# Kernel tuning notes

Measured on AMD Instinct MI355X. Metric: run time of the kernel, lower is better.

Reference implementation:

```python
import jax, jax.numpy as jnp
import numpy as np

N = 100000
E = 1600000
IN_C, HID_C, OUT_C = 128, 128, 64
EPS = 1e-5


def setup_inputs() -> dict:
    key = jax.random.key(0)
    ks = jax.random.split(key, 12)
    x = jax.random.normal(ks[0], (N, IN_C), dtype=jnp.float32)
    edge_index = jax.random.randint(ks[1], (2, E), 0, N, dtype=jnp.int64)
    def lin(k, fan_in, fan_out):
        s = 1.0 / np.sqrt(fan_in)
        return jax.random.uniform(k, (fan_in, fan_out), jnp.float32, -s, s)
    return {
        "x": x,
        "W1": lin(ks[2], IN_C, HID_C), "b1": jnp.zeros((HID_C,), jnp.float32),
        "g1": jnp.ones((HID_C,), jnp.float32), "be1": jnp.zeros((HID_C,), jnp.float32),
        "W2": lin(ks[3], HID_C, HID_C), "b2": jnp.zeros((HID_C,), jnp.float32),
        "g2": jnp.ones((HID_C,), jnp.float32), "be2": jnp.zeros((HID_C,), jnp.float32),
        "W3": lin(ks[4], HID_C, OUT_C), "b3": jnp.zeros((OUT_C,), jnp.float32),
        "edge_index": edge_index,
    }


def gcn_conv(x, W, b, src, dst, dinv):
    # x' = D^{-1/2}(A+I)D^{-1/2} (x W) + b ; src/dst already include self loops
    h = x @ W                                    # [N, C_out]
    norm = dinv[src] * dinv[dst]                 # [E+N]
    msg = h[src] * norm[:, None]                 # [E+N, C_out] (memory-bound gather)
    out = jax.ops.segment_sum(msg, dst, num_segments=N)
    return out + b


def batchnorm_relu(h, gamma, beta):
    # training-mode BatchNorm1d: batch stats over nodes, biased variance
    mean = jnp.mean(h, axis=0)
    var = jnp.mean((h - mean) ** 2, axis=0)
    y = gamma * (h - mean) * jax.lax.rsqrt(var + EPS) + beta
    return jax.nn.relu(y)


def reference(x, W1, b1, g1, be1, W2, b2, g2, be2, W3, b3, edge_index):
    loop = jnp.arange(N, dtype=edge_index.dtype)
    src = jnp.concatenate([edge_index[0], loop])
    dst = jnp.concatenate([edge_index[1], loop])
    deg = jax.ops.segment_sum(jnp.ones_like(dst, dtype=jnp.float32), dst, num_segments=N)
    dinv = jax.lax.rsqrt(jnp.maximum(deg, 1.0))

    h = gcn_conv(x, W1, b1, src, dst, dinv)
    h = batchnorm_relu(h, g1, be1)
    h = gcn_conv(h, W2, b2, src, dst, dinv)
    h = batchnorm_relu(h, g2, be2)
    out = gcn_conv(h, W3, b3, src, dst, dinv)
    return (h, out)
```

## Files before the change

### kernel.cpp

```cpp
#include <hip/hip_runtime.h>
#include <hip/hip_bf16.h>

#define NNODES 100000
#define NEDGES 1600000
#define EPSBN 1e-5f

#define BKT_SHIFT 9
#define NODES_PER_BKT 512
#define NBKT 196
#define NCHUNK 256
#define CHUNK 6250
#define SRC_MASK 0x1FFFF
#define NSLOT 64

typedef unsigned short u16;
typedef unsigned int u32;
typedef __bf16 bf16x8 __attribute__((ext_vector_type(8)));
typedef float floatx4 __attribute__((ext_vector_type(4)));
typedef unsigned int uint4v __attribute__((ext_vector_type(4)));
typedef float float4v __attribute__((ext_vector_type(4)));

__device__ __forceinline__ u16 f2bf(float f) {
    unsigned int u = __float_as_uint(f);
    unsigned int r = (u + 0x7fffu + ((u >> 16) & 1u)) >> 16;
    return (u16)r;
}
__device__ __forceinline__ float bflo(unsigned int u) { return __uint_as_float(u << 16); }
__device__ __forceinline__ float bfhi(unsigned int u) { return __uint_as_float(u & 0xffff0000u); }

__device__ __forceinline__ void nt_store_u4(void* p, uint4 v) {
    uint4v t; t.x = v.x; t.y = v.y; t.z = v.z; t.w = v.w;
    __builtin_nontemporal_store(t, (uint4v*)p);
}
__device__ __forceinline__ void nt_store_f4(float* p, float4 v) {
    float4v t; t.x = v.x; t.y = v.y; t.z = v.z; t.w = v.w;
    __builtin_nontemporal_store(t, (float4v*)p);
}


__global__ __launch_bounds__(256) void k_hist(const int* __restrict__ ei, int* __restrict__ histT) {
    __shared__ int h[NBKT];
    int tid = threadIdx.x;
    if (tid < NBKT) h[tid] = 0;
    __syncthreads();
    int base = blockIdx.x * CHUNK;
    for (int e = base + tid; e < base + CHUNK; e += 256) {
        int d = ei[NEDGES + e];
        atomicAdd(&h[d >> BKT_SHIFT], 1);
    }
    __syncthreads();
    if (tid < NBKT) histT[tid * NCHUNK + blockIdx.x] = h[tid];
}

__global__ __launch_bounds__(256) void k_bbase(const int* __restrict__ histT, int* __restrict__ bbase,
                                               int* __restrict__ rowptr) {
    __shared__ int sdata[256];
    int tid = threadIdx.x;
    int s = 0;
    if (tid < NBKT) {
        for (int g = 0; g < NCHUNK; ++g) s += histT[tid * NCHUNK + g];
    }
    int val = s;
    sdata[tid] = val;
    __syncthreads();
    for (int off = 1; off < 256; off <<= 1) {
        int add = (tid >= off) ? sdata[tid - off] : 0;
        __syncthreads();
        val += add;
        sdata[tid] = val;
        __syncthreads();
    }
    if (tid < NBKT) bbase[tid] = val - s;
    if (tid == 0) { bbase[NBKT] = NEDGES; rowptr[NNODES] = NEDGES; }
}

__global__ __launch_bounds__(256) void k_bscan(const int* __restrict__ histT, const int* __restrict__ bbase,
                                               int* __restrict__ offT) {
    __shared__ int sdata[256];
    int b = blockIdx.x;
    int g = threadIdx.x;
    int v = histT[b * NCHUNK + g];
    int val = v;
    sdata[g] = val;
    __syncthreads();
    for (int off = 1; off < 256; off <<= 1) {
        int add = (g >= off) ? sdata[g - off] : 0;
        __syncthreads();
        val += add;
        sdata[g] = val;
        __syncthreads();
    }
    offT[b * NCHUNK + g] = bbase[b] + (val - v);
}

__global__ __launch_bounds__(256) void k_scatter(const int* __restrict__ ei, const int* __restrict__ offT,
                                                 u32* __restrict__ rec) {
    __shared__ int cur[NBKT];
    int tid = threadIdx.x;
    if (tid < NBKT) cur[tid] = offT[tid * NCHUNK + blockIdx.x];
    __syncthreads();
    int base = blockIdx.x * CHUNK;
    for (int e = base + tid; e < base + CHUNK; e += 256) {
        int s = ei[e];
        int d = ei[NEDGES + e];
        int b = d >> BKT_SHIFT;
        int p = atomicAdd(&cur[b], 1);
        rec[p] = ((u32)(d & (NODES_PER_BKT - 1)) << 17) | (u32)s;
    }
}

__global__ __launch_bounds__(256) void k_bfill(const u32* __restrict__ rec, const int* __restrict__ bbase,
                                               int* __restrict__ rowptr, float* __restrict__ dinv,
                                               int* __restrict__ colsrc) {
    __shared__ int cnt[NODES_PER_BKT];
    __shared__ int sdata[256];
    int tid = threadIdx.x;
    int b = blockIdx.x;
    int n0 = b * NODES_PER_BKT;
    int r0 = bbase[b], r1 = bbase[b + 1];
    cnt[2 * tid] = 0;
    cnt[2 * tid + 1] = 0;
    __syncthreads();
    for (int r = r0 + tid; r < r1; r += 256) {
        atomicAdd(&cnt[rec[r] >> 17], 1);
    }
    __syncthreads();
    int c0 = cnt[2 * tid], c1 = cnt[2 * tid + 1];
    int ps = c0 + c1;
    int val = ps;
    sdata[tid] = val;
    __syncthreads();
    for (int off = 1; off < 256; off <<= 1) {
        int add = (tid >= off) ? sdata[tid - off] : 0;
        __syncthreads();
        val += add;
        sdata[tid] = val;
        __syncthreads();
    }
    int e0 = val - ps;
    int e1 = e0 + c0;
    int na = n0 + 2 * tid, nb2 = n0 + 2 * tid + 1;
    if (na < NNODES) {
        rowptr[na] = r0 + e0;
        dinv[na] = rsqrtf((float)(c0 + 1));
    }
    if (nb2 < NNODES) {
        rowptr[nb2] = r0 + e1;
        dinv[nb2] = rsqrtf((float)(c1 + 1));
    }
    cnt[2 * tid] = r0 + e0;
    cnt[2 * tid + 1] = r0 + e1;
    __syncthreads();
    for (int r = r0 + tid; r < r1; r += 256) {
        u32 u = rec[r];
        int p = atomicAdd(&cnt[u >> 17], 1);
        colsrc[p] = (int)(u & SRC_MASK);
    }
}


template <int COUT>
__device__ __forceinline__ void packone(const float* __restrict__ W, u16* __restrict__ Wp, int f) {
    constexpr int CT = COUT / 16;
    if (f >= 4 * CT * 64) return;
    int ks = f / (CT * 64);
    int ct = (f / 64) % CT;
    int lane = f % 64;
    int quad = lane >> 4, mm = lane & 15;
#pragma unroll
    for (int j = 0; j < 8; ++j) {
        float v = W[(size_t)(ks * 32 + quad * 8 + j) * COUT + ct * 16 + mm];
        Wp[(size_t)f * 8 + j] = f2bf(v);
    }
}

__global__ __launch_bounds__(256) void k_packW_all(const float* __restrict__ W1, const float* __restrict__ W2,
                                                   const float* __restrict__ W3, u16* __restrict__ Wp1,
                                                   u16* __restrict__ Wp2, u16* __restrict__ Wp3) {
    int b = blockIdx.x;
    if (b < 8) packone<128>(W1, Wp1, b * 256 + threadIdx.x);
    else if (b < 16) packone<128>(W2, Wp2, (b - 8) * 256 + threadIdx.x);
    else packone<64>(W3, Wp3, (b - 16) * 256 + threadIdx.x);
}


template <int COUT, bool AFFINE, bool WRITEH, bool BF16IN>
__global__ __launch_bounds__(256) void k_mfma_gemm(const void* __restrict__ Xv, const u16* __restrict__ Wp,
                                                   const float* __restrict__ dinv,
                                                   const float* __restrict__ scale, const float* __restrict__ shift,
                                                   u16* __restrict__ Bout, float* __restrict__ Hout) {
    constexpr int CT = COUT / 16;
    const int wave = threadIdx.x >> 6;
    const int lane = threadIdx.x & 63;
    const int quad = lane >> 4;
    const int m = lane & 15;
    const int rowbase = blockIdx.x * 64 + wave * 16;
    const int arow = rowbase + m;
    const bool rv = arow < NNODES;
    floatx4 acc[CT];
#pragma unroll
    for (int ct = 0; ct < CT; ++ct) acc[ct] = floatx4{0.f, 0.f, 0.f, 0.f};
#pragma unroll
    for (int ks = 0; ks < 4; ++ks) {
        const int k0 = ks * 32 + quad * 8;
        float4 xa = make_float4(0.f, 0.f, 0.f, 0.f), xb = xa;
        if (rv) {
            if (BF16IN) {
                uint4 q = *(const uint4*)((const u16*)Xv + (size_t)arow * 128 + k0);
                xa.x = bflo(q.x); xa.y = bfhi(q.x); xa.z = bflo(q.y); xa.w = bfhi(q.y);
                xb.x = bflo(q.z); xb.y = bfhi(q.z); xb.z = bflo(q.w); xb.w = bfhi(q.w);
            } else {
                xa = *(const float4*)((const float*)Xv + (size_t)arow * 128 + k0);
                xb = *(const float4*)((const float*)Xv + (size_t)arow * 128 + k0 + 4);
            }
        }
        if (AFFINE) {
            float4 sa = *(const float4*)(scale + k0), sb = *(const float4*)(scale + k0 + 4);
            float4 ha = *(const float4*)(shift + k0), hb = *(const float4*)(shift + k0 + 4);
            xa.x = fmaxf(fmaf(xa.x, sa.x, ha.x), 0.f);
            xa.y = fmaxf(fmaf(xa.y, sa.y, ha.y), 0.f);
            xa.z = fmaxf(fmaf(xa.z, sa.z, ha.z), 0.f);
            xa.w = fmaxf(fmaf(xa.w, sa.w, ha.w), 0.f);
            xb.x = fmaxf(fmaf(xb.x, sb.x, hb.x), 0.f);
            xb.y = fmaxf(fmaf(xb.y, sb.y, hb.y), 0.f);
            xb.z = fmaxf(fmaf(xb.z, sb.z, hb.z), 0.f);
            xb.w = fmaxf(fmaf(xb.w, sb.w, hb.w), 0.f);
        }
        if (WRITEH && rv) {
            nt_store_f4(Hout + (size_t)arow * 128 + k0, xa);
            nt_store_f4(Hout + (size_t)arow * 128 + k0 + 4, xb);
        }
        union { u16 h[8]; bf16x8 v; } ua;
        ua.h[0] = f2bf(xa.x); ua.h[1] = f2bf(xa.y); ua.h[2] = f2bf(xa.z); ua.h[3] = f2bf(xa.w);
        ua.h[4] = f2bf(xb.x); ua.h[5] = f2bf(xb.y); ua.h[6] = f2bf(xb.z); ua.h[7] = f2bf(xb.w);
#pragma unroll
        for (int ct = 0; ct < CT; ++ct) {
            uint4 bv = *(const uint4*)(Wp + ((size_t)(ks * CT + ct) * 64 + lane) * 8);
            bf16x8 b = *(const bf16x8*)&bv;
            acc[ct] = __builtin_amdgcn_mfma_f32_16x16x32_bf16(ua.v, b, acc[ct], 0, 0, 0);
        }
    }
    float dv[4];
#pragma unroll
    for (int reg = 0; reg < 4; ++reg) {
        int r = rowbase + quad * 4 + reg;
        dv[reg] = (r < NNODES) ? dinv[r] : 0.f;
    }
#pragma unroll
    for (int ct = 0; ct < CT; ++ct) {
#pragma unroll
        for (int reg = 0; reg < 4; ++reg) {
            int r = rowbase + quad * 4 + reg;
            if (r < NNODES) Bout[(size_t)r * COUT + ct * 16 + m] = f2bf(dv[reg] * acc[ct][reg]);
        }
    }
}


template <bool STATS, bool OUTB>
__global__ __launch_bounds__(256) void k_agg128v(const u16* __restrict__ Bm, const float* __restrict__ dinv,
                                                 const int* __restrict__ rowptr, const int* __restrict__ colsrc,
                                                 const float* __restrict__ bias, void* __restrict__ Outv,
                                                 float* __restrict__ slots) {
    __shared__ float sO[4][128];
    const int wave = threadIdx.x >> 6;
    const int node = blockIdx.x * 4 + wave;
    const int lane = threadIdx.x & 63;
    const int g = lane >> 4;
    const int c16 = lane & 15;
    const uint4* Bq = (const uint4*)Bm;
    float a0[8], a1[8];
#pragma unroll
    for (int j = 0; j < 8; ++j) { a0[j] = 0.f; a1[j] = 0.f; }
    const int beg = rowptr[node];
    const int L = rowptr[node + 1] - beg + 1;
    for (int it = 0; it < L; it += 8) {
        int i0 = it + g, i1 = it + 4 + g;
        float w0 = (i0 < L) ? 1.f : 0.f;
        float w1 = (i1 < L) ? 1.f : 0.f;
        i0 = min(i0, L - 1);
        i1 = min(i1, L - 1);
        int s0 = colsrc[beg + max(i0, 1) - 1];
        int s1 = colsrc[beg + max(i1, 1) - 1];
        if (i0 == 0) s0 = node;
        uint4 q0 = Bq[(size_t)s0 * 16 + c16];
        uint4 q1 = Bq[(size_t)s1 * 16 + c16];
        a0[0] += w0 * bflo(q0.x); a0[1] += w0 * bfhi(q0.x);
        a0[2] += w0 * bflo(q0.y); a0[3] += w0 * bfhi(q0.y);
        a0[4] += w0 * bflo(q0.z); a0[5] += w0 * bfhi(q0.z);
        a0[6] += w0 * bflo(q0.w); a0[7] += w0 * bfhi(q0.w);
        a1[0] += w1 * bflo(q1.x); a1[1] += w1 * bfhi(q1.x);
        a1[2] += w1 * bflo(q1.y); a1[3] += w1 * bfhi(q1.y);
        a1[4] += w1 * bflo(q1.z); a1[5] += w1 * bfhi(q1.z);
        a1[6] += w1 * bflo(q1.w); a1[7] += w1 * bfhi(q1.w);
    }
    const float dv = dinv[node];
    float o[8];
#pragma unroll
    for (int j = 0; j < 8; ++j) {
        float s = a0[j] + a1[j];
        s += __shfl_xor(s, 16);
        s += __shfl_xor(s, 32);
        o[j] = dv * s + bias[c16 * 8 + j];
    }
    if (g == 0) {
        if (OUTB) {
            u16* OutB = (u16*)Outv;
            union { u32 w[4]; uint4 q; } p;
            p.w[0] = (u32)f2bf(o[0]) | ((u32)f2bf(o[1]) << 16);
            p.w[1] = (u32)f2bf(o[2]) | ((u32)f2bf(o[3]) << 16);
            p.w[2] = (u32)f2bf(o[4]) | ((u32)f2bf(o[5]) << 16);
            p.w[3] = (u32)f2bf(o[6]) | ((u32)f2bf(o[7]) << 16);
            nt_store_u4(OutB + (size_t)node * 128 + c16 * 8, p.q);
        } else {
            float* Out = (float*)Outv;
            nt_store_f4(Out + (size_t)node * 128 + c16 * 8, make_float4(o[0], o[1], o[2], o[3]));
            nt_store_f4(Out + (size_t)node * 128 + c16 * 8 + 4, make_float4(o[4], o[5], o[6], o[7]));
        }
        if (STATS) {
#pragma unroll
            for (int j = 0; j < 8; ++j) sO[wave][c16 * 8 + j] = o[j];
        }
    }
    if (STATS) {
        __syncthreads();
        if (threadIdx.x < 128) {
            float s = 0.f, q = 0.f;
#pragma unroll
            for (int wv = 0; wv < 4; ++wv) {
                float v = sO[wv][threadIdx.x];
                s += v;
                q += v * v;
            }
            float* slot = slots + (size_t)(blockIdx.x & (NSLOT - 1)) * 256;
            atomicAdd(&slot[threadIdx.x], s);
            atomicAdd(&slot[128 + threadIdx.x], q);
        }
    }
}

__global__ __launch_bounds__(256) void k_agg64v(const u16* __restrict__ Bm, const float* __restrict__ dinv,
                                                const int* __restrict__ rowptr, const int* __restrict__ colsrc,
                                                const float* __restrict__ bias, float* __restrict__ Out) {
    const int node = blockIdx.x * 4 + (threadIdx.x >> 6);
    const int lane = threadIdx.x & 63;
    const int g = lane >> 3;
    const int c8 = lane & 7;
    const uint4* Bq = (const uint4*)Bm;
    float a0[8], a1[8];
#pragma unroll
    for (int j = 0; j < 8; ++j) { a0[j] = 0.f; a1[j] = 0.f; }
    const int beg = rowptr[node];
    const int L = rowptr[node + 1] - beg + 1;
    for (int it = 0; it < L; it += 16) {
        int i0 = it + g, i1 = it + 8 + g;
        float w0 = (i0 < L) ? 1.f : 0.f;
        float w1 = (i1 < L) ? 1.f : 0.f;
        i0 = min(i0, L - 1);
        i1 = min(i1, L - 1);
        int s0 = colsrc[beg + max(i0, 1) - 1];
        int s1 = colsrc[beg + max(i1, 1) - 1];
        if (i0 == 0) s0 = node;
        uint4 q0 = Bq[(size_t)s0 * 8 + c8];
        uint4 q1 = Bq[(size_t)s1 * 8 + c8];
        a0[0] += w0 * bflo(q0.x); a0[1] += w0 * bfhi(q0.x);
        a0[2] += w0 * bflo(q0.y); a0[3] += w0 * bfhi(q0.y);
        a0[4] += w0 * bflo(q0.z); a0[5] += w0 * bfhi(q0.z);
        a0[6] += w0 * bflo(q0.w); a0[7] += w0 * bfhi(q0.w);
        a1[0] += w1 * bflo(q1.x); a1[1] += w1 * bfhi(q1.x);
        a1[2] += w1 * bflo(q1.y); a1[3] += w1 * bfhi(q1.y);
        a1[4] += w1 * bflo(q1.z); a1[5] += w1 * bfhi(q1.z);
        a1[6] += w1 * bflo(q1.w); a1[7] += w1 * bfhi(q1.w);
    }
    const float dv = dinv[node];
    float o[8];
#pragma unroll
    for (int j = 0; j < 8; ++j) {
        float s = a0[j] + a1[j];
        s += __shfl_xor(s, 8);
        s += __shfl_xor(s, 16);
        s += __shfl_xor(s, 32);
        o[j] = dv * s + bias[c8 * 8 + j];
    }
    if (g == 0) {
        nt_store_f4(Out + (size_t)node * 64 + c8 * 8, make_float4(o[0], o[1], o[2], o[3]));
        nt_store_f4(Out + (size_t)node * 64 + c8 * 8 + 4, make_float4(o[4], o[5], o[6], o[7]));
    }
}


__global__ void k_bn_final(const float* __restrict__ slots, const float* __restrict__ g,
                           const float* __restrict__ be, float* __restrict__ scale, float* __restrict__ shift) {
    int c = threadIdx.x;
    float s = 0.f, q = 0.f;
    for (int k = 0; k < NSLOT; ++k) {
        s += slots[(size_t)k * 256 + c];
        q += slots[(size_t)k * 256 + 128 + c];
    }
    float mean = s * (1.0f / NNODES);
    float var = q * (1.0f / NNODES) - mean * mean;
    float istd = rsqrtf(var + EPSBN);
    float sc = g[c] * istd;
    scale[c] = sc;
    shift[c] = be[c] - sc * mean;
}


extern "C" void kernel_launch(void* const* d_in, const int* in_sizes, int n_in,
                              void* d_out, int out_size, void* d_ws, size_t ws_size,
                              hipStream_t stream) {
    const float* x   = (const float*)d_in[0];
    const float* W1  = (const float*)d_in[1];
    const float* b1  = (const float*)d_in[2];
    const float* g1  = (const float*)d_in[3];
    const float* be1 = (const float*)d_in[4];
    const float* W2  = (const float*)d_in[5];
    const float* b2  = (const float*)d_in[6];
    const float* g2  = (const float*)d_in[7];
    const float* be2 = (const float*)d_in[8];
    const float* W3  = (const float*)d_in[9];
    const float* b3  = (const float*)d_in[10];
    const int* ei    = (const int*)d_in[11];

    float* out_h = (float*)d_out;
    float* out_o = (float*)d_out + (size_t)NNODES * 128;

    char* w = (char*)d_ws;
    u16* A16 = (u16*)w;        w += (size_t)NNODES * 128 * 2;
    u16* Bm = (u16*)w;         w += (size_t)NNODES * 128 * 2;
    float* dinv = (float*)w;   w += (size_t)NNODES * 4;
    int* rowptr = (int*)w;     w += (size_t)(NNODES + 32) * 4;
    int* colsrc = (int*)w;     w += (size_t)(NEDGES + 8) * 4;
    int* bbase = (int*)w;      w += (NBKT + 4) * 4;
    float* slots1 = (float*)w; w += (size_t)NSLOT * 256 * 4;
    float* slots2 = (float*)w; w += (size_t)NSLOT * 256 * 4;
    float* scale = (float*)w;  w += 128 * 4;
    float* shift = (float*)w;  w += 128 * 4;
    u16* Wp1 = (u16*)w;        w += 128 * 128 * 2;
    u16* Wp2 = (u16*)w;        w += 128 * 128 * 2;
    u16* Wp3 = (u16*)w;        w += 128 * 64 * 2;

    u32* rec  = (u32*)A16;
    int* histT = (int*)Bm;
    int* offT  = (int*)Bm + NBKT * NCHUNK;

    hipMemsetAsync(slots1, 0, (size_t)2 * NSLOT * 256 * 4, stream);

    k_packW_all<<<20, 256, 0, stream>>>(W1, W2, W3, Wp1, Wp2, Wp3);

    k_hist<<<NCHUNK, 256, 0, stream>>>(ei, histT);
    k_bbase<<<1, 256, 0, stream>>>(histT, bbase, rowptr);
    k_bscan<<<NBKT, 256, 0, stream>>>(histT, bbase, offT);
    k_scatter<<<NCHUNK, 256, 0, stream>>>(ei, offT, rec);
    k_bfill<<<NBKT, 256, 0, stream>>>(rec, bbase, rowptr, dinv, colsrc);

    const int GB = (NNODES + 63) / 64;
    const int AB = NNODES / 4;

    k_mfma_gemm<128, false, false, false><<<GB, 256, 0, stream>>>(x, Wp1, dinv, nullptr, nullptr, Bm, nullptr);
    k_agg128v<true, true><<<AB, 256, 0, stream>>>(Bm, dinv, rowptr, colsrc, b1, A16, slots1);
    k_bn_final<<<1, 128, 0, stream>>>(slots1, g1, be1, scale, shift);

    k_mfma_gemm<128, true, false, true><<<GB, 256, 0, stream>>>(A16, Wp2, dinv, scale, shift, Bm, nullptr);
    k_agg128v<true, true><<<AB, 256, 0, stream>>>(Bm, dinv, rowptr, colsrc, b2, A16, slots2);
    k_bn_final<<<1, 128, 0, stream>>>(slots2, g2, be2, scale, shift);

    k_mfma_gemm<64, true, true, true><<<GB, 256, 0, stream>>>(A16, Wp3, dinv, scale, shift, Bm, out_h);
    k_agg64v<<<AB, 256, 0, stream>>>(Bm, dinv, rowptr, colsrc, b3, out_o);
}
```

Baseline: 463.5 us.

## Split 128-wide aggregation into two 64-column halves per block

The 128-channel aggregation kernel now launches twice as many blocks. Each block handles one 64-column half for four nodes, and the two halves of a node group sit in adjacent block IDs so they can share cache for the gathered rows. Each wave now processes 16 edges per iteration instead of 8, which is meant to raise memory-level parallelism on the gather. Index loads from colsrc are made nontemporal. In exchange, colsrc and rowptr are read twice and there are more BN-stat atomics per node.

```diff
diff --git a/kernel.cpp b/kernel.cpp
--- a/kernel.cpp
+++ b/kernel.cpp
@@ -258,33 +258,37 @@
 
 
 template <bool STATS, bool OUTB>
-__global__ __launch_bounds__(256) void k_agg128v(const u16* __restrict__ Bm, const float* __restrict__ dinv,
+__global__ __launch_bounds__(256) void k_agg128h(const u16* __restrict__ Bm, const float* __restrict__ dinv,
                                                  const int* __restrict__ rowptr, const int* __restrict__ colsrc,
                                                  const float* __restrict__ bias, void* __restrict__ Outv,
                                                  float* __restrict__ slots) {
-    __shared__ float sO[4][128];
+    __shared__ float sO[4][64];
+    const int bid = blockIdx.x;
+    const int half = (bid & 7) >> 2;
+    const int nodeblk = (bid >> 3) * 4 + (bid & 3);
     const int wave = threadIdx.x >> 6;
-    const int node = blockIdx.x * 4 + wave;
+    const int node = nodeblk * 4 + wave;
     const int lane = threadIdx.x & 63;
-    const int g = lane >> 4;
-    const int c16 = lane & 15;
+    const int g = lane >> 3;
+    const int c8 = lane & 7;
     const uint4* Bq = (const uint4*)Bm;
+    const int hoff = half * 8 + c8;
     float a0[8], a1[8];
 #pragma unroll
     for (int j = 0; j < 8; ++j) { a0[j] = 0.f; a1[j] = 0.f; }
     const int beg = rowptr[node];
     const int L = rowptr[node + 1] - beg + 1;
-    for (int it = 0; it < L; it += 8) {
-        int i0 = it + g, i1 = it + 4 + g;
+    for (int it = 0; it < L; it += 16) {
+        int i0 = it + g, i1 = it + 8 + g;
         float w0 = (i0 < L) ? 1.f : 0.f;
         float w1 = (i1 < L) ? 1.f : 0.f;
         i0 = min(i0, L - 1);
         i1 = min(i1, L - 1);
-        int s0 = colsrc[beg + max(i0, 1) - 1];
-        int s1 = colsrc[beg + max(i1, 1) - 1];
+        int s0 = __builtin_nontemporal_load(&colsrc[beg + max(i0, 1) - 1]);
+        int s1 = __builtin_nontemporal_load(&colsrc[beg + max(i1, 1) - 1]);
         if (i0 == 0) s0 = node;
-        uint4 q0 = Bq[(size_t)s0 * 16 + c16];
-        uint4 q1 = Bq[(size_t)s1 * 16 + c16];
+        uint4 q0 = Bq[(size_t)s0 * 16 + hoff];
+        uint4 q1 = Bq[(size_t)s1 * 16 + hoff];
         a0[0] += w0 * bflo(q0.x); a0[1] += w0 * bfhi(q0.x);
         a0[2] += w0 * bflo(q0.y); a0[3] += w0 * bfhi(q0.y);
         a0[4] += w0 * bflo(q0.z); a0[5] += w0 * bfhi(q0.z);
@@ -299,9 +303,10 @@
 #pragma unroll
     for (int j = 0; j < 8; ++j) {
         float s = a0[j] + a1[j];
+        s += __shfl_xor(s, 8);
         s += __shfl_xor(s, 16);
         s += __shfl_xor(s, 32);
-        o[j] = dv * s + bias[c16 * 8 + j];
+        o[j] = dv * s + bias[half * 64 + c8 * 8 + j];
     }
     if (g == 0) {
         if (OUTB) {
@@ -311,20 +316,20 @@
             p.w[1] = (u32)f2bf(o[2]) | ((u32)f2bf(o[3]) << 16);
             p.w[2] = (u32)f2bf(o[4]) | ((u32)f2bf(o[5]) << 16);
             p.w[3] = (u32)f2bf(o[6]) | ((u32)f2bf(o[7]) << 16);
-            nt_store_u4(OutB + (size_t)node * 128 + c16 * 8, p.q);
+            nt_store_u4(OutB + (size_t)node * 128 + half * 64 + c8 * 8, p.q);
         } else {
             float* Out = (float*)Outv;
-            nt_store_f4(Out + (size_t)node * 128 + c16 * 8, make_float4(o[0], o[1], o[2], o[3]));
-            nt_store_f4(Out + (size_t)node * 128 + c16 * 8 + 4, make_float4(o[4], o[5], o[6], o[7]));
+            nt_store_f4(Out + (size_t)node * 128 + half * 64 + c8 * 8, make_float4(o[0], o[1], o[2], o[3]));
+            nt_store_f4(Out + (size_t)node * 128 + half * 64 + c8 * 8 + 4, make_float4(o[4], o[5], o[6], o[7]));
         }
         if (STATS) {
 #pragma unroll
-            for (int j = 0; j < 8; ++j) sO[wave][c16 * 8 + j] = o[j];
+            for (int j = 0; j < 8; ++j) sO[wave][c8 * 8 + j] = o[j];
         }
     }
     if (STATS) {
         __syncthreads();
-        if (threadIdx.x < 128) {
+        if (threadIdx.x < 64) {
             float s = 0.f, q = 0.f;
 #pragma unroll
             for (int wv = 0; wv < 4; ++wv) {
@@ -332,9 +337,9 @@
                 s += v;
                 q += v * v;
             }
-            float* slot = slots + (size_t)(blockIdx.x & (NSLOT - 1)) * 256;
-            atomicAdd(&slot[threadIdx.x], s);
-            atomicAdd(&slot[128 + threadIdx.x], q);
+            float* slot = slots + (size_t)(bid & (NSLOT - 1)) * 256;
+            atomicAdd(&slot[half * 64 + threadIdx.x], s);
+            atomicAdd(&slot[128 + half * 64 + threadIdx.x], q);
         }
     }
 }
@@ -358,8 +363,8 @@
         float w1 = (i1 < L) ? 1.f : 0.f;
         i0 = min(i0, L - 1);
         i1 = min(i1, L - 1);
-        int s0 = colsrc[beg + max(i0, 1) - 1];
-        int s1 = colsrc[beg + max(i1, 1) - 1];
+        int s0 = __builtin_nontemporal_load(&colsrc[beg + max(i0, 1) - 1]);
+        int s1 = __builtin_nontemporal_load(&colsrc[beg + max(i1, 1) - 1]);
         if (i0 == 0) s0 = node;
         uint4 q0 = Bq[(size_t)s0 * 8 + c8];
         uint4 q1 = Bq[(size_t)s1 * 8 + c8];
@@ -456,13 +461,14 @@
 
     const int GB = (NNODES + 63) / 64;
     const int AB = NNODES / 4;
+    const int AB2 = 2 * AB;
 
     k_mfma_gemm<128, false, false, false><<<GB, 256, 0, stream>>>(x, Wp1, dinv, nullptr, nullptr, Bm, nullptr);
-    k_agg128v<true, true><<<AB, 256, 0, stream>>>(Bm, dinv, rowptr, colsrc, b1, A16, slots1);
+    k_agg128h<true, true><<<AB2, 256, 0, stream>>>(Bm, dinv, rowptr, colsrc, b1, A16, slots1);
     k_bn_final<<<1, 128, 0, stream>>>(slots1, g1, be1, scale, shift);
 
     k_mfma_gemm<128, true, false, true><<<GB, 256, 0, stream>>>(A16, Wp2, dinv, scale, shift, Bm, nullptr);
-    k_agg128v<true, true><<<AB, 256, 0, stream>>>(Bm, dinv, rowptr, colsrc, b2, A16, slots2);
+    k_agg128h<true, true><<<AB2, 256, 0, stream>>>(Bm, dinv, rowptr, colsrc, b2, A16, slots2);
     k_bn_final<<<1, 128, 0, stream>>>(slots2, g2, be2, scale, shift);
 
     k_mfma_gemm<64, true, true, true><<<GB, 256, 0, stream>>>(A16, Wp3, dinv, scale, shift, Bm, out_h);
```

Result: slower. 528.3 us (+14.0%).
